# Kernel optimization log

Measured on AMD Instinct MI355X. Metric: run time of the kernel, lower is better.

## Reference

```python
import jax, jax.numpy as jnp
import numpy as np

CUTOFF = 1.0          # nm, PhysNet attenuation cutoff
KE = 138.96           # Coulomb constant in kJ/mol*nm/e^2
N_ATOMS = 245760
N_PAIRS = 16_777_216
N_MOLS = 4096


def physnet_attenuation(r):
    # PhysNet smooth cutoff: 1 - 6u^5 + 15u^4 - 10u^3 for u = r/cutoff < 1, else 0
    u = r / CUTOFF
    phi = 1.0 - 6.0 * u**5 + 15.0 * u**4 - 10.0 * u**3
    return jnp.where(u < 1.0, phi, 0.0)


def setup_inputs() -> dict:
    key = jax.random.key(0)
    k1, k2, k3, k4 = jax.random.split(key, 4)
    per_atom_charge = jax.random.normal(k1, (N_ATOMS,), dtype=jnp.float32) * 0.2
    raw = jax.random.randint(k2, (2, N_PAIRS), 0, N_ATOMS, dtype=jnp.int32)
    # enforce idx_i <= idx_j; equal pairs are dropped by the idx_i < idx_j mask
    pair_indices = jnp.stack([jnp.minimum(raw[0], raw[1]), jnp.maximum(raw[0], raw[1])])
    # distances in (0.05, 1.5) nm to avoid div-by-zero and span the cutoff
    d_ij = jax.random.uniform(k3, (N_PAIRS, 1), dtype=jnp.float32) * 1.45 + 0.05
    atomic_subsystem_indices = jax.random.randint(k4, (N_PAIRS,), 0, N_MOLS, dtype=jnp.int32)
    per_system_energy = jnp.zeros((N_MOLS,), dtype=jnp.float32)
    return {
        "per_atom_charge": per_atom_charge,
        "pair_indices": pair_indices,
        "d_ij": d_ij,
        "atomic_subsystem_indices": atomic_subsystem_indices,
        "per_system_energy": per_system_energy,
    }


def reference(per_atom_charge, pair_indices, d_ij, atomic_subsystem_indices, per_system_energy):
    idx_i = pair_indices[0]
    idx_j = pair_indices[1]
    unique_mask = idx_i < idx_j  # keep each pair once (static-shape masking via where)
    d = d_ij[:, 0]  # [P]
    phi_2r = physnet_attenuation(2.0 * d)
    # cutoff-blended Coulomb kernel chi(r)
    chi_r = phi_2r / jnp.sqrt(d * d + 1.0) + (1.0 - phi_2r) / d
    contrib = per_atom_charge[idx_i] * per_atom_charge[idx_j] * chi_r
    contrib = jnp.where(unique_mask, contrib, 0.0)
    energy = per_system_energy + jax.ops.segment_sum(
        contrib, atomic_subsystem_indices, num_segments=N_MOLS
    )
    return energy * KE
```

## Files before the change

kernel.cpp:

```cpp
#include <hip/hip_runtime.h>

static constexpr int   NPAIRS = 16777216;
static constexpr int   NMOLS  = 4096;
static constexpr float KEF    = 138.96f;
static constexpr int   TPB    = 256;
static constexpr int   BLOCKS = 2048;
static constexpr int   WAVES  = TPB / 64;
static constexpr int   NITER  = NPAIRS / 4 / (BLOCKS * TPB);

typedef int   vi4 __attribute__((ext_vector_type(4)));
typedef float vf4 __attribute__((ext_vector_type(4)));

__global__ __launch_bounds__(256) void zero_out_kernel(float* __restrict__ out) {
    int i = blockIdx.x * 256 + threadIdx.x;
    if (i < NMOLS) out[i] = 0.0f;
}

__device__ __forceinline__ void stage16(const void* gptr, void* lptr) {
    __builtin_amdgcn_global_load_lds((const unsigned int*)gptr, (unsigned int*)lptr,
                                     16, 0, 0);
}

__device__ __forceinline__ float pair_contrib(const float* __restrict__ q,
                                              int i, int j, float d) {
    float u = 2.0f * d;
    float phi = 0.0f;
    if (u < 1.0f) {
        phi = 1.0f - u * u * u * (10.0f + u * (6.0f * u - 15.0f));
    }
    float rs = __builtin_amdgcn_rsqf(d * d + 1.0f);
    float rd = __builtin_amdgcn_rcpf(d);
    float chi = phi * rs + (1.0f - phi) * rd;
    float c = q[i] * q[j] * chi;
    return (i < j) ? c : 0.0f;
}

__global__ __launch_bounds__(TPB) void coulomb_kernel(
    const float* __restrict__ q,
    const int*   __restrict__ pidx,
    const float* __restrict__ dij,
    const int*   __restrict__ mol,
    float*       __restrict__ out)
{
    __shared__ float bins[NMOLS];
    __shared__ vi4   stage[WAVES][4][64];
    for (int i = threadIdx.x; i < NMOLS; i += TPB) bins[i] = 0.0f;
    __syncthreads();

    const vi4* pi4 = (const vi4*)pidx;
    const vi4* pj4 = (const vi4*)(pidx + NPAIRS);
    const vf4* d4  = (const vf4*)dij;
    const vi4* m4  = (const vi4*)mol;

    const int lane   = threadIdx.x & 63;
    const int wave   = threadIdx.x >> 6;
    const int stride = BLOCKS * TPB;
    int v = blockIdx.x * TPB + threadIdx.x;

    #pragma unroll 1
    for (int k = 0; k < NITER; ++k, v += stride) {
        stage16(&pi4[v], &stage[wave][0][0]);
        stage16(&pj4[v], &stage[wave][1][0]);
        stage16(&d4[v],  &stage[wave][2][0]);
        stage16(&m4[v],  &stage[wave][3][0]);
        asm volatile("s_waitcnt vmcnt(0)" ::: "memory");

        vi4 ii = stage[wave][0][lane];
        vi4 jj = stage[wave][1][lane];
        vf4 dd = (vf4)stage[wave][2][lane];
        vi4 mm = stage[wave][3][lane];

        float c0 = pair_contrib(q, ii.x, jj.x, dd.x);
        float c1 = pair_contrib(q, ii.y, jj.y, dd.y);
        float c2 = pair_contrib(q, ii.z, jj.z, dd.z);
        float c3 = pair_contrib(q, ii.w, jj.w, dd.w);

        atomicAdd(&bins[mm.x], c0);
        atomicAdd(&bins[mm.y], c1);
        atomicAdd(&bins[mm.z], c2);
        atomicAdd(&bins[mm.w], c3);
    }

    __syncthreads();
    for (int i = threadIdx.x; i < NMOLS; i += TPB) {
        atomicAdd(&out[i], bins[i]);
    }
}

__global__ __launch_bounds__(256) void finalize_kernel(float* __restrict__ out,
                                                       const float* __restrict__ pse) {
    int i = blockIdx.x * 256 + threadIdx.x;
    if (i < NMOLS) out[i] = (out[i] + pse[i]) * KEF;
}

extern "C" void kernel_launch(void* const* d_in, const int* in_sizes, int n_in,
                              void* d_out, int out_size, void* d_ws, size_t ws_size,
                              hipStream_t stream) {
    const float* q    = (const float*)d_in[0];
    const int*   pidx = (const int*)  d_in[1];
    const float* dij  = (const float*)d_in[2];
    const int*   mol  = (const int*)  d_in[3];
    const float* pse  = (const float*)d_in[4];
    float* out = (float*)d_out;

    zero_out_kernel<<<NMOLS / 256, 256, 0, stream>>>(out);
    coulomb_kernel<<<BLOCKS, TPB, 0, stream>>>(q, pidx, dij, mol, out);
    finalize_kernel<<<NMOLS / 256, 256, 0, stream>>>(out, pse);
}
```

Baseline: 381.0 us.

## Unroll pair loads with nontemporal vectors and cache low-index charges in LDS

Replaces per-iteration LDS staging with direct nontemporal vector loads unrolled four deep. This raises the number of memory requests in flight and removes the full vmcnt wait each iteration. It also caches the first 24576 charges as bf16 in shared memory to skip some global gathers, and halves the block count. The bf16 cache adds rounding error for those charges and a per-block preload, and the larger LDS footprint may lower occupancy.

```diff
diff --git a/kernel.cpp b/kernel.cpp
--- a/kernel.cpp
+++ b/kernel.cpp
@@ -2,11 +2,12 @@
 
 static constexpr int   NPAIRS = 16777216;
 static constexpr int   NMOLS  = 4096;
+static constexpr int   NCACHE = 24576;
 static constexpr float KEF    = 138.96f;
 static constexpr int   TPB    = 256;
-static constexpr int   BLOCKS = 2048;
-static constexpr int   WAVES  = TPB / 64;
+static constexpr int   BLOCKS = 1024;
 static constexpr int   NITER  = NPAIRS / 4 / (BLOCKS * TPB);
+static constexpr int   UNROLL = 4;
 
 typedef int   vi4 __attribute__((ext_vector_type(4)));
 typedef float vf4 __attribute__((ext_vector_type(4)));
@@ -16,22 +17,30 @@
     if (i < NMOLS) out[i] = 0.0f;
 }
 
-__device__ __forceinline__ void stage16(const void* gptr, void* lptr) {
-    __builtin_amdgcn_global_load_lds((const unsigned int*)gptr, (unsigned int*)lptr,
-                                     16, 0, 0);
+__device__ __forceinline__ unsigned short f2bf(float f) {
+    unsigned u = __float_as_uint(f);
+    u += 0x7fffu + ((u >> 16) & 1u);
+    return (unsigned short)(u >> 16);
+}
+__device__ __forceinline__ float bf2f(unsigned short h) {
+    return __uint_as_float(((unsigned)h) << 16);
 }
 
-__device__ __forceinline__ float pair_contrib(const float* __restrict__ q,
+__device__ __forceinline__ float getq(const float* __restrict__ q,
+                                      const unsigned short* qc, int idx) {
+    return (idx < NCACHE) ? bf2f(qc[idx]) : q[idx];
+}
+
+__device__ __forceinline__ float pair_contrib(float qi, float qj,
                                               int i, int j, float d) {
     float u = 2.0f * d;
     float phi = 0.0f;
     if (u < 1.0f) {
         phi = 1.0f - u * u * u * (10.0f + u * (6.0f * u - 15.0f));
     }
-    float rs = __builtin_amdgcn_rsqf(d * d + 1.0f);
-    float rd = __builtin_amdgcn_rcpf(d);
-    float chi = phi * rs + (1.0f - phi) * rd;
-    float c = q[i] * q[j] * chi;
+    float chi = phi * __builtin_amdgcn_rsqf(d * d + 1.0f)
+              + (1.0f - phi) * __builtin_amdgcn_rcpf(d);
+    float c = qi * qj * chi;
     return (i < j) ? c : 0.0f;
 }
 
@@ -42,9 +51,20 @@
     const int*   __restrict__ mol,
     float*       __restrict__ out)
 {
-    __shared__ float bins[NMOLS];
-    __shared__ vi4   stage[WAVES][4][64];
+    __shared__ float          bins[NMOLS];
+    __shared__ unsigned short qc[NCACHE];
+
     for (int i = threadIdx.x; i < NMOLS; i += TPB) bins[i] = 0.0f;
+    {
+        const vf4* q4 = (const vf4*)q;
+        for (int i = threadIdx.x; i < NCACHE / 4; i += TPB) {
+            vf4 qq = q4[i];
+            qc[4 * i + 0] = f2bf(qq.x);
+            qc[4 * i + 1] = f2bf(qq.y);
+            qc[4 * i + 2] = f2bf(qq.z);
+            qc[4 * i + 3] = f2bf(qq.w);
+        }
+    }
     __syncthreads();
 
     const vi4* pi4 = (const vi4*)pidx;
@@ -52,33 +72,45 @@
     const vf4* d4  = (const vf4*)dij;
     const vi4* m4  = (const vi4*)mol;
 
-    const int lane   = threadIdx.x & 63;
-    const int wave   = threadIdx.x >> 6;
     const int stride = BLOCKS * TPB;
     int v = blockIdx.x * TPB + threadIdx.x;
 
     #pragma unroll 1
-    for (int k = 0; k < NITER; ++k, v += stride) {
-        stage16(&pi4[v], &stage[wave][0][0]);
-        stage16(&pj4[v], &stage[wave][1][0]);
-        stage16(&d4[v],  &stage[wave][2][0]);
-        stage16(&m4[v],  &stage[wave][3][0]);
-        asm volatile("s_waitcnt vmcnt(0)" ::: "memory");
-
-        vi4 ii = stage[wave][0][lane];
-        vi4 jj = stage[wave][1][lane];
-        vf4 dd = (vf4)stage[wave][2][lane];
-        vi4 mm = stage[wave][3][lane];
-
-        float c0 = pair_contrib(q, ii.x, jj.x, dd.x);
-        float c1 = pair_contrib(q, ii.y, jj.y, dd.y);
-        float c2 = pair_contrib(q, ii.z, jj.z, dd.z);
-        float c3 = pair_contrib(q, ii.w, jj.w, dd.w);
-
-        atomicAdd(&bins[mm.x], c0);
-        atomicAdd(&bins[mm.y], c1);
-        atomicAdd(&bins[mm.z], c2);
-        atomicAdd(&bins[mm.w], c3);
+    for (int k = 0; k < NITER; k += UNROLL) {
+        vi4 ii[UNROLL], jj[UNROLL], mm[UNROLL];
+        vf4 dd[UNROLL];
+        #pragma unroll
+        for (int t = 0; t < UNROLL; ++t) {
+            int va = v + t * stride;
+            ii[t] = __builtin_nontemporal_load(&pi4[va]);
+            jj[t] = __builtin_nontemporal_load(&pj4[va]);
+            dd[t] = __builtin_nontemporal_load(&d4[va]);
+            mm[t] = __builtin_nontemporal_load(&m4[va]);
+        }
+        float qi[UNROLL][4], qj[UNROLL][4];
+        #pragma unroll
+        for (int t = 0; t < UNROLL; ++t) {
+            qi[t][0] = getq(q, qc, ii[t].x);
+            qi[t][1] = getq(q, qc, ii[t].y);
+            qi[t][2] = getq(q, qc, ii[t].z);
+            qi[t][3] = getq(q, qc, ii[t].w);
+            qj[t][0] = getq(q, qc, jj[t].x);
+            qj[t][1] = getq(q, qc, jj[t].y);
+            qj[t][2] = getq(q, qc, jj[t].z);
+            qj[t][3] = getq(q, qc, jj[t].w);
+        }
+        #pragma unroll
+        for (int t = 0; t < UNROLL; ++t) {
+            float c0 = pair_contrib(qi[t][0], qj[t][0], ii[t].x, jj[t].x, dd[t].x);
+            float c1 = pair_contrib(qi[t][1], qj[t][1], ii[t].y, jj[t].y, dd[t].y);
+            float c2 = pair_contrib(qi[t][2], qj[t][2], ii[t].z, jj[t].z, dd[t].z);
+            float c3 = pair_contrib(qi[t][3], qj[t][3], ii[t].w, jj[t].w, dd[t].w);
+            atomicAdd(&bins[mm[t].x], c0);
+            atomicAdd(&bins[mm[t].y], c1);
+            atomicAdd(&bins[mm[t].z], c2);
+            atomicAdd(&bins[mm[t].w], c3);
+        }
+        v += UNROLL * stride;
     }
 
     __syncthreads();
```

Measured after the change: 405.3 us. 1.06x slower.
